# Performance work log

Measured on AMD Instinct MI355X. Metric: run time of the kernel, lower is better.

Reference implementation:

```python
import jax, jax.numpy as jnp
import numpy as np

N = 20000        # nodes
E = 320000       # directed edges (before self-loops)
HEADS = 4
IN_DIM = 256
HID = [256, 128]
ZD = [128, 64]
S = 10           # num_samples in reparameterize
REAL_MIN = 2.2e-10
THETA_MAX = 1000.0
KMIN, KMAX = 0.1, 1000.0
SLOPE = 0.2      # GATConv leaky_relu negative_slope


def setup_inputs() -> dict:
    key = jax.random.key(0)
    ks = jax.random.split(key, 24)
    f32 = jnp.float32
    def p(k, shape, scale):
        return jax.random.normal(k, shape, dtype=f32) * scale
    inp = {}
    inp["x"] = jax.random.normal(ks[0], (N, IN_DIM), dtype=f32)
    inp["edge_index"] = jax.random.randint(ks[1], (2, E), 0, N)
    # layer 0: GAT 256 -> 4 heads x 64 (concat = 256)
    inp["gatW0"] = p(ks[2], (HID[0], IN_DIM), 0.06)
    inp["asrc0"] = p(ks[3], (HEADS, HID[0] // HEADS), 0.1)
    inp["adst0"] = p(ks[4], (HEADS, HID[0] // HEADS), 0.1)
    inp["gatb0"] = p(ks[5], (HID[0],), 0.02)
    inp["fcW0"] = p(ks[6], (ZD[0], HID[0]), 0.06)
    inp["fcb0"] = p(ks[7], (ZD[0],), 0.02)
    inp["shW0"] = p(ks[8], (ZD[0], ZD[0]), 0.08)
    inp["shb0"] = p(ks[9], (ZD[0],), 0.02)
    inp["scW0"] = p(ks[10], (ZD[0], ZD[0]), 0.08)
    inp["scb0"] = p(ks[11], (ZD[0],), 0.02)
    # layer 1: GAT 256 -> 4 heads x 32 (concat = 128)
    inp["gatW1"] = p(ks[12], (HID[1], HID[0]), 0.06)
    inp["asrc1"] = p(ks[13], (HEADS, HID[1] // HEADS), 0.1)
    inp["adst1"] = p(ks[14], (HEADS, HID[1] // HEADS), 0.1)
    inp["gatb1"] = p(ks[15], (HID[1],), 0.02)
    inp["fcW1"] = p(ks[16], (ZD[1], HID[1]), 0.06)
    inp["fcb1"] = p(ks[17], (ZD[1],), 0.02)
    inp["shW1"] = p(ks[18], (ZD[1], ZD[1]), 0.08)
    inp["shb1"] = p(ks[19], (ZD[1],), 0.02)
    inp["scW1"] = p(ks[20], (ZD[1], ZD[1]), 0.08)
    inp["scb1"] = p(ks[21], (ZD[1],), 0.02)
    # Weibull reparameterization noise eps ~ U(0,1), shape (S, z_dim, N)
    inp["eps0"] = jax.random.uniform(ks[22], (S, ZD[0], N), dtype=f32)
    inp["eps1"] = jax.random.uniform(ks[23], (S, ZD[1], N), dtype=f32)
    return inp


def _gat(x, src, dst, W, a_src, a_dst, b):
    """PyG GATConv (shared lin, concat heads, add_self_loops done by caller)."""
    n = x.shape[0]
    xw = (x @ W.T).reshape(n, HEADS, -1)            # [N, H, C]
    s = (xw * a_src[None]).sum(-1)                  # [N, H] alpha_src
    d = (xw * a_dst[None]).sum(-1)                  # [N, H] alpha_dst
    e = s[src] + d[dst]                             # [E, H]
    e = jnp.where(e > 0, e, SLOPE * e)              # leaky_relu
    m = jax.lax.stop_gradient(jax.ops.segment_max(e, dst, num_segments=n))
    ex = jnp.exp(e - m[dst])
    den = jax.ops.segment_sum(ex, dst, num_segments=n)
    alpha = ex / (den[dst] + 1e-16)                 # segment softmax over in-edges
    out = jax.ops.segment_sum(alpha[:, :, None] * xw[src], dst, num_segments=n)
    return out.reshape(n, -1) + b                   # [N, H*C]


def _reparam(k, l, eps):
    # theta = l * (-log(max(1-eps, real_min)))^(1/k), mean over samples, clamp
    lm = jnp.log(jnp.maximum(1.0 - eps, REAL_MIN))  # [S, z, N]
    theta = l[None] * jnp.power(-lm, 1.0 / k[None])
    return jnp.clip(theta.mean(0), REAL_MIN, THETA_MAX)


def _right(h, Wk, bk, Wl, bl, eps):
    k = jnp.clip(jax.nn.softplus(h @ Wk.T + bk).T, KMIN, KMAX)      # [z, N]
    l = jnp.maximum(jax.nn.softplus(h @ Wl.T + bl).T, REAL_MIN)     # [z, N]
    l = l / jnp.exp(jax.lax.lgamma(1.0 + 1.0 / k))
    return _reparam(k, l, eps), k, l


def reference(x, edge_index, gatW0, asrc0, adst0, gatb0, fcW0, fcb0, shW0, shb0,
              scW0, scb0, gatW1, asrc1, adst1, gatb1, fcW1, fcb1, shW1, shb1,
              scW1, scb1, eps0, eps1):
    n = x.shape[0]
    loops = jnp.arange(n)
    src = jnp.concatenate([edge_index[0], loops])   # GATConv add_self_loops
    dst = jnp.concatenate([edge_index[1], loops])
    h0 = _gat(x, src, dst, gatW0, asrc0, adst0, gatb0)
    z0 = jax.nn.softplus(h0 @ fcW0.T + fcb0)
    h1 = _gat(h0, src, dst, gatW1, asrc1, adst1, gatb1)
    z1 = jax.nn.softplus(h1 @ fcW1.T + fcb1)
    theta1, k1, l1 = _right(z1, shW1, shb1, scW1, scb1, eps1)
    theta0, k0, l0 = _right(z0, shW0, shb0, scW0, scb0, eps0)
    return (theta0, theta1, k0, k1, l0, l1)
```

## Files before the change

### kernel.cpp

```cpp
#include <hip/hip_runtime.h>
#include <math.h>

#define N_NODES 20000
#define E_EDGES 320000
#define NHEADS 4
#define RMIN 2.2e-10f
#define THETA_MAX 1000.0f
#define SLOPE 0.2f

__device__ __forceinline__ float softplus_f(float x) {
    return fmaxf(x, 0.0f) + log1pf(expf(-fabsf(x)));
}

__global__ __launch_bounds__(256) void count_kernel(const int* __restrict__ dst,
                                                    int* __restrict__ deg) {
    int e = blockIdx.x * 256 + threadIdx.x;
    if (e < E_EDGES) atomicAdd(&deg[dst[e]], 1);
}

__global__ __launch_bounds__(256) void scan_kernel(const int* __restrict__ deg,
                                                   int* __restrict__ rowptr,
                                                   int* __restrict__ cursor) {
    __shared__ int part[256];
    int t = threadIdx.x;
    const int CH = (N_NODES + 255) / 256;
    int base = t * CH;
    int sum = 0;
    for (int i = 0; i < CH; ++i) {
        int idx = base + i;
        if (idx < N_NODES) sum += deg[idx];
    }
    part[t] = sum;
    __syncthreads();
    for (int off = 1; off < 256; off <<= 1) {
        int v = (t >= off) ? part[t - off] : 0;
        __syncthreads();
        part[t] += v;
        __syncthreads();
    }
    int run = (t == 0) ? 0 : part[t - 1];
    for (int i = 0; i < CH; ++i) {
        int idx = base + i;
        if (idx < N_NODES) {
            rowptr[idx] = run;
            cursor[idx] = run;
            run += deg[idx];
        }
    }
    if (t == 255) rowptr[N_NODES] = run;
}

__global__ __launch_bounds__(256) void scatter_kernel(const int* __restrict__ src,
                                                      const int* __restrict__ dst,
                                                      int* __restrict__ cursor,
                                                      int* __restrict__ csr) {
    int e = blockIdx.x * 256 + threadIdx.x;
    if (e < E_EDGES) {
        int p = atomicAdd(&cursor[dst[e]], 1);
        csr[p] = src[e];
    }
}

template <int MODE, bool TRANS>
__global__ __launch_bounds__(256) void gemm_kernel(const float* __restrict__ A,
                                                   const float* __restrict__ W,
                                                   const float* __restrict__ bias,
                                                   float* __restrict__ out,
                                                   int M, int K, int NO) {
    __shared__ float As[16][68];
    __shared__ float Bs[16][68];
    int tid = threadIdx.x;
    int tx = tid & 15, ty = tid >> 4;
    int bm = blockIdx.x * 64;
    int bn = blockIdx.y * 64;
    float acc[4][4] = {};
    for (int k0 = 0; k0 < K; k0 += 16) {
        {
            int m = tid >> 2;
            int kk0 = (tid & 3) * 4;
            int row = bm + m;
            float4 v = make_float4(0.f, 0.f, 0.f, 0.f);
            if (row < M) v = *(const float4*)(A + (size_t)row * K + k0 + kk0);
            As[kk0 + 0][m] = v.x; As[kk0 + 1][m] = v.y;
            As[kk0 + 2][m] = v.z; As[kk0 + 3][m] = v.w;
        }
        {
            int o = tid >> 2;
            int kk0 = (tid & 3) * 4;
            float4 v = *(const float4*)(W + (size_t)(bn + o) * K + k0 + kk0);
            Bs[kk0 + 0][o] = v.x; Bs[kk0 + 1][o] = v.y;
            Bs[kk0 + 2][o] = v.z; Bs[kk0 + 3][o] = v.w;
        }
        __syncthreads();
#pragma unroll
        for (int kk = 0; kk < 16; ++kk) {
            float a[4], b[4];
            *(float4*)a = *(const float4*)(&As[kk][ty * 4]);
            *(float4*)b = *(const float4*)(&Bs[kk][tx * 4]);
#pragma unroll
            for (int i = 0; i < 4; ++i)
#pragma unroll
                for (int j = 0; j < 4; ++j) acc[i][j] += a[i] * b[j];
        }
        __syncthreads();
    }
    int r0 = bm + ty * 4;
    int c0 = bn + tx * 4;
    float bv[4] = {0.f, 0.f, 0.f, 0.f};
    if (MODE != 0) *(float4*)bv = *(const float4*)(bias + c0);
    float vals[4][4];
#pragma unroll
    for (int i = 0; i < 4; ++i)
#pragma unroll
        for (int j = 0; j < 4; ++j) {
            float v = acc[i][j];
            if (MODE == 1) v = softplus_f(v + bv[j]);
            else if (MODE == 2) { v = softplus_f(v + bv[j]); v = fminf(fmaxf(v, 0.1f), 1000.0f); }
            else if (MODE == 3) { v = fmaxf(softplus_f(v + bv[j]), RMIN); }
            vals[i][j] = v;
        }
    if (!TRANS) {
#pragma unroll
        for (int i = 0; i < 4; ++i) {
            int row = r0 + i;
            if (row < M) *(float4*)(out + (size_t)row * NO + c0) = *(float4*)vals[i];
        }
    } else {
        if (r0 + 3 < M) {
#pragma unroll
            for (int j = 0; j < 4; ++j) {
                float col[4] = {vals[0][j], vals[1][j], vals[2][j], vals[3][j]};
                *(float4*)(out + (size_t)(c0 + j) * M + r0) = *(float4*)col;
            }
        } else {
#pragma unroll
            for (int i = 0; i < 4; ++i) {
                int row = r0 + i;
                if (row < M)
#pragma unroll
                    for (int j = 0; j < 4; ++j) out[(size_t)(c0 + j) * M + row] = vals[i][j];
            }
        }
    }
}

template <int F, int CPER>
__global__ __launch_bounds__(256) void sd_kernel(const float* __restrict__ xw,
                                                 const float* __restrict__ asrc,
                                                 const float* __restrict__ adst,
                                                 float* __restrict__ s,
                                                 float* __restrict__ d) {
    int wave = threadIdx.x >> 6;
    int lane = threadIdx.x & 63;
    int n = blockIdx.x * 4 + wave;
    if (n >= N_NODES) return;
    float ss[NHEADS] = {0, 0, 0, 0}, dd[NHEADS] = {0, 0, 0, 0};
#pragma unroll
    for (int j = 0; j < F / 64; ++j) {
        int c = j * 64 + lane;
        int h = c / CPER;
        int cc = c % CPER;
        float v = xw[(size_t)n * F + c];
        ss[h] += v * asrc[h * CPER + cc];
        dd[h] += v * adst[h * CPER + cc];
    }
#pragma unroll
    for (int off = 32; off > 0; off >>= 1) {
#pragma unroll
        for (int h = 0; h < NHEADS; ++h) {
            ss[h] += __shfl_xor(ss[h], off, 64);
            dd[h] += __shfl_xor(dd[h], off, 64);
        }
    }
    if (lane == 0) {
#pragma unroll
        for (int h = 0; h < NHEADS; ++h) {
            s[n * NHEADS + h] = ss[h];
            d[n * NHEADS + h] = dd[h];
        }
    }
}

template <int F, int CPER>
__global__ __launch_bounds__(256) void agg_kernel(const float* __restrict__ xw,
                                                  const float* __restrict__ s,
                                                  const float* __restrict__ d,
                                                  const int* __restrict__ rowptr,
                                                  const int* __restrict__ csr,
                                                  const float* __restrict__ bias,
                                                  float* __restrict__ out) {
    int wave = threadIdx.x >> 6;
    int lane = threadIdx.x & 63;
    int n = blockIdx.x * 4 + wave;
    if (n >= N_NODES) return;
    constexpr int J = F / 64;
    float dh[NHEADS], shh[NHEADS];
#pragma unroll
    for (int h = 0; h < NHEADS; ++h) {
        dh[h] = d[n * NHEADS + h];
        shh[h] = s[n * NHEADS + h];
    }
    float den[NHEADS], w[NHEADS], acc[J];
#pragma unroll
    for (int h = 0; h < NHEADS; ++h) {
        float e = shh[h] + dh[h];
        e = e > 0.f ? e : SLOPE * e;
        w[h] = expf(e);
        den[h] = w[h];
    }
#pragma unroll
    for (int j = 0; j < J; ++j) {
        int c = j * 64 + lane;
        acc[j] = w[c / CPER] * xw[(size_t)n * F + c];
    }
    int beg = rowptr[n], end = rowptr[n + 1];
    for (int idx = beg; idx < end; ++idx) {
        int srcn = csr[idx];
#pragma unroll
        for (int h = 0; h < NHEADS; ++h) {
            float e = s[srcn * NHEADS + h] + dh[h];
            e = e > 0.f ? e : SLOPE * e;
            w[h] = expf(e);
            den[h] += w[h];
        }
#pragma unroll
        for (int j = 0; j < J; ++j) {
            int c = j * 64 + lane;
            acc[j] += w[c / CPER] * xw[(size_t)srcn * F + c];
        }
    }
#pragma unroll
    for (int j = 0; j < J; ++j) {
        int c = j * 64 + lane;
        out[(size_t)n * F + c] = acc[j] / (den[c / CPER] + 1e-16f) + bias[c];
    }
}

__global__ __launch_bounds__(256) void theta_kernel(const float* __restrict__ eps,
                                                    const float* __restrict__ kptr,
                                                    float* __restrict__ lptr,
                                                    float* __restrict__ theta, int ZN) {
    int i = blockIdx.x * 256 + threadIdx.x;
    if (i >= ZN) return;
    float k = kptr[i];
    float invk = 1.0f / k;
    float lg = expf(lgammaf(1.0f + invk));
    float l = lptr[i] / lg;
    lptr[i] = l;
    float acc = 0.0f;
#pragma unroll
    for (int ss = 0; ss < 10; ++ss) {
        float u = eps[(size_t)ss * ZN + i];
        float v = -logf(fmaxf(1.0f - u, RMIN));
        acc += exp2f(log2f(v) * invk);
    }
    float th = l * acc * 0.1f;
    th = fminf(fmaxf(th, RMIN), THETA_MAX);
    theta[i] = th;
}

extern "C" void kernel_launch(void* const* d_in, const int* in_sizes, int n_in,
                              void* d_out, int out_size, void* d_ws, size_t ws_size,
                              hipStream_t stream) {
    const float* x     = (const float*)d_in[0];
    const int*   eidx  = (const int*)d_in[1];
    const float* gatW0 = (const float*)d_in[2];
    const float* asrc0 = (const float*)d_in[3];
    const float* adst0 = (const float*)d_in[4];
    const float* gatb0 = (const float*)d_in[5];
    const float* fcW0  = (const float*)d_in[6];
    const float* fcb0  = (const float*)d_in[7];
    const float* shW0  = (const float*)d_in[8];
    const float* shb0  = (const float*)d_in[9];
    const float* scW0  = (const float*)d_in[10];
    const float* scb0  = (const float*)d_in[11];
    const float* gatW1 = (const float*)d_in[12];
    const float* asrc1 = (const float*)d_in[13];
    const float* adst1 = (const float*)d_in[14];
    const float* gatb1 = (const float*)d_in[15];
    const float* fcW1  = (const float*)d_in[16];
    const float* fcb1  = (const float*)d_in[17];
    const float* shW1  = (const float*)d_in[18];
    const float* shb1  = (const float*)d_in[19];
    const float* scW1  = (const float*)d_in[20];
    const float* scb1  = (const float*)d_in[21];
    const float* eps0  = (const float*)d_in[22];
    const float* eps1  = (const float*)d_in[23];

    const int* e_src = eidx;
    const int* e_dst = eidx + E_EDGES;

    size_t off = 0;
    auto carve = [&](size_t elems) {
        void* p = (char*)d_ws + off;
        off += ((elems * 4 + 255) / 256) * 256;
        return p;
    };
    float* xw0 = (float*)carve(20000u * 256);
    float* h0  = (float*)carve(20000u * 256);
    float* z0  = (float*)carve(20000u * 128);
    float* xw1 = (float*)carve(20000u * 128);
    float* h1  = (float*)carve(20000u * 128);
    float* z1  = (float*)carve(20000u * 64);
    float* s0  = (float*)carve(20000u * 4);
    float* d0  = (float*)carve(20000u * 4);
    float* s1  = (float*)carve(20000u * 4);
    float* d1  = (float*)carve(20000u * 4);
    int* deg    = (int*)carve(20000);
    int* rowptr = (int*)carve(20001);
    int* cursor = (int*)carve(20000);
    int* csr    = (int*)carve(E_EDGES);

    float* out    = (float*)d_out;
    float* theta0 = out;
    float* theta1 = out + 2560000;
    float* k0     = out + 3840000;
    float* k1     = out + 6400000;
    float* l0     = out + 7680000;
    float* l1     = out + 10240000;

    const int M = N_NODES;
    dim3 blk(256);

    (void)hipMemsetAsync(deg, 0, N_NODES * sizeof(int), stream);
    count_kernel<<<(E_EDGES + 255) / 256, blk, 0, stream>>>(e_dst, deg);
    scan_kernel<<<1, blk, 0, stream>>>(deg, rowptr, cursor);
    scatter_kernel<<<(E_EDGES + 255) / 256, blk, 0, stream>>>(e_src, e_dst, cursor, csr);

    gemm_kernel<0, false><<<dim3(313, 4), blk, 0, stream>>>(x, gatW0, nullptr, xw0, M, 256, 256);
    sd_kernel<256, 64><<<5000, blk, 0, stream>>>(xw0, asrc0, adst0, s0, d0);
    agg_kernel<256, 64><<<5000, blk, 0, stream>>>(xw0, s0, d0, rowptr, csr, gatb0, h0);
    gemm_kernel<1, false><<<dim3(313, 2), blk, 0, stream>>>(h0, fcW0, fcb0, z0, M, 256, 128);

    gemm_kernel<0, false><<<dim3(313, 2), blk, 0, stream>>>(h0, gatW1, nullptr, xw1, M, 256, 128);
    sd_kernel<128, 32><<<5000, blk, 0, stream>>>(xw1, asrc1, adst1, s1, d1);
    agg_kernel<128, 32><<<5000, blk, 0, stream>>>(xw1, s1, d1, rowptr, csr, gatb1, h1);
    gemm_kernel<1, false><<<dim3(313, 1), blk, 0, stream>>>(h1, fcW1, fcb1, z1, M, 128, 64);

    gemm_kernel<2, true><<<dim3(313, 2), blk, 0, stream>>>(z0, shW0, shb0, k0, M, 128, 128);
    gemm_kernel<3, true><<<dim3(313, 2), blk, 0, stream>>>(z0, scW0, scb0, l0, M, 128, 128);
    gemm_kernel<2, true><<<dim3(313, 1), blk, 0, stream>>>(z1, shW1, shb1, k1, M, 64, 64);
    gemm_kernel<3, true><<<dim3(313, 1), blk, 0, stream>>>(z1, scW1, scb1, l1, M, 64, 64);

    theta_kernel<<<(2560000 + 255) / 256, blk, 0, stream>>>(eps0, k0, l0, theta0, 2560000);
    theta_kernel<<<(1280000 + 255) / 256, blk, 0, stream>>>(eps1, k1, l1, theta1, 1280000);
}
```

Measured before the change: 684.0 us.

## Precompute per-edge attention weights in separate kernel and unroll aggregation by two

Adds an edge-weight kernel that computes leaky-relu and exp attention weights for every CSR edge and self-loop once, storing them as float4 per edge. The scatter step now also records each edge's destination in CSR order. The aggregation kernel reads these precomputed weights instead of recomputing exp per head on every lane, and processes two neighbours per iteration to expose more memory-level parallelism. In exchange it adds an extra launch and about 5 MB of weight traffic per layer.

```diff
diff --git a/kernel.cpp b/kernel.cpp
--- a/kernel.cpp
+++ b/kernel.cpp
@@ -53,12 +53,45 @@
 __global__ __launch_bounds__(256) void scatter_kernel(const int* __restrict__ src,
                                                       const int* __restrict__ dst,
                                                       int* __restrict__ cursor,
-                                                      int* __restrict__ csr) {
+                                                      int* __restrict__ csr,
+                                                      int* __restrict__ dnd) {
     int e = blockIdx.x * 256 + threadIdx.x;
     if (e < E_EDGES) {
-        int p = atomicAdd(&cursor[dst[e]], 1);
+        int dn = dst[e];
+        int p = atomicAdd(&cursor[dn], 1);
         csr[p] = src[e];
-    }
+        dnd[p] = dn;
+    }
+}
+
+__global__ __launch_bounds__(256) void eweight_kernel(const int* __restrict__ csr,
+                                                      const int* __restrict__ dnd,
+                                                      const float* __restrict__ s,
+                                                      const float* __restrict__ d,
+                                                      float* __restrict__ w4,
+                                                      float* __restrict__ wself) {
+    int p = blockIdx.x * 256 + threadIdx.x;
+    if (p >= E_EDGES + N_NODES) return;
+    int sn, dn;
+    float* outp;
+    if (p < E_EDGES) {
+        sn = csr[p];
+        dn = dnd[p];
+        outp = w4 + 4 * (size_t)p;
+    } else {
+        sn = p - E_EDGES;
+        dn = sn;
+        outp = wself + 4 * (size_t)sn;
+    }
+    float4 sv = *(const float4*)(s + 4 * (size_t)sn);
+    float4 dv = *(const float4*)(d + 4 * (size_t)dn);
+    float4 wv;
+    float e;
+    e = sv.x + dv.x; e = e > 0.f ? e : SLOPE * e; wv.x = expf(e);
+    e = sv.y + dv.y; e = e > 0.f ? e : SLOPE * e; wv.y = expf(e);
+    e = sv.z + dv.z; e = e > 0.f ? e : SLOPE * e; wv.z = expf(e);
+    e = sv.w + dv.w; e = e > 0.f ? e : SLOPE * e; wv.w = expf(e);
+    *(float4*)outp = wv;
 }
 
 template <int MODE, bool TRANS>
@@ -181,12 +214,23 @@
     }
 }
 
+template <int CPER>
+__device__ __forceinline__ float pick_w(float4 w, int j, int lane) {
+    if constexpr (CPER == 64) {
+        return j == 0 ? w.x : (j == 1 ? w.y : (j == 2 ? w.z : w.w));
+    } else {
+        float lo = (j == 0) ? w.x : w.z;
+        float hi = (j == 0) ? w.y : w.w;
+        return (lane & 32) ? hi : lo;
+    }
+}
+
 template <int F, int CPER>
 __global__ __launch_bounds__(256) void agg_kernel(const float* __restrict__ xw,
-                                                  const float* __restrict__ s,
-                                                  const float* __restrict__ d,
                                                   const int* __restrict__ rowptr,
                                                   const int* __restrict__ csr,
+                                                  const float* __restrict__ w4,
+                                                  const float* __restrict__ wself,
                                                   const float* __restrict__ bias,
                                                   float* __restrict__ out) {
     int wave = threadIdx.x >> 6;
@@ -194,45 +238,57 @@
     int n = blockIdx.x * 4 + wave;
     if (n >= N_NODES) return;
     constexpr int J = F / 64;
-    float dh[NHEADS], shh[NHEADS];
-#pragma unroll
-    for (int h = 0; h < NHEADS; ++h) {
-        dh[h] = d[n * NHEADS + h];
-        shh[h] = s[n * NHEADS + h];
-    }
-    float den[NHEADS], w[NHEADS], acc[J];
-#pragma unroll
-    for (int h = 0; h < NHEADS; ++h) {
-        float e = shh[h] + dh[h];
-        e = e > 0.f ? e : SLOPE * e;
-        w[h] = expf(e);
-        den[h] = w[h];
-    }
+
+    float4 wl = *(const float4*)(wself + 4 * (size_t)n);
+    float den[NHEADS] = {wl.x, wl.y, wl.z, wl.w};
+    float acc[J];
 #pragma unroll
     for (int j = 0; j < J; ++j) {
         int c = j * 64 + lane;
-        acc[j] = w[c / CPER] * xw[(size_t)n * F + c];
-    }
+        acc[j] = pick_w<CPER>(wl, j, lane) * xw[(size_t)n * F + c];
+    }
+
     int beg = rowptr[n], end = rowptr[n + 1];
-    for (int idx = beg; idx < end; ++idx) {
-        int srcn = csr[idx];
-#pragma unroll
-        for (int h = 0; h < NHEADS; ++h) {
-            float e = s[srcn * NHEADS + h] + dh[h];
-            e = e > 0.f ? e : SLOPE * e;
-            w[h] = expf(e);
-            den[h] += w[h];
-        }
+    int idx = beg;
+    for (; idx + 2 <= end; idx += 2) {
+        int sa = csr[idx], sb = csr[idx + 1];
+        float4 wa = *(const float4*)(w4 + 4 * (size_t)idx);
+        float4 wb = *(const float4*)(w4 + 4 * (size_t)(idx + 1));
+        den[0] += wa.x + wb.x;
+        den[1] += wa.y + wb.y;
+        den[2] += wa.z + wb.z;
+        den[3] += wa.w + wb.w;
+        const float* ra = xw + (size_t)sa * F;
+        const float* rb = xw + (size_t)sb * F;
 #pragma unroll
         for (int j = 0; j < J; ++j) {
             int c = j * 64 + lane;
-            acc[j] += w[c / CPER] * xw[(size_t)srcn * F + c];
-        }
-    }
+            acc[j] += pick_w<CPER>(wa, j, lane) * ra[c];
+            acc[j] += pick_w<CPER>(wb, j, lane) * rb[c];
+        }
+    }
+    if (idx < end) {
+        int sa = csr[idx];
+        float4 wa = *(const float4*)(w4 + 4 * (size_t)idx);
+        den[0] += wa.x;
+        den[1] += wa.y;
+        den[2] += wa.z;
+        den[3] += wa.w;
+        const float* ra = xw + (size_t)sa * F;
+#pragma unroll
+        for (int j = 0; j < J; ++j) {
+            int c = j * 64 + lane;
+            acc[j] += pick_w<CPER>(wa, j, lane) * ra[c];
+        }
+    }
+
 #pragma unroll
     for (int j = 0; j < J; ++j) {
         int c = j * 64 + lane;
-        out[(size_t)n * F + c] = acc[j] / (den[c / CPER] + 1e-16f) + bias[c];
+        float dv;
+        if constexpr (CPER == 64) dv = den[j];
+        else dv = (lane & 32) ? den[2 * j + 1] : den[2 * j];
+        out[(size_t)n * F + c] = acc[j] / (dv + 1e-16f) + bias[c];
     }
 }
 
@@ -310,6 +366,9 @@
     int* rowptr = (int*)carve(20001);
     int* cursor = (int*)carve(20000);
     int* csr    = (int*)carve(E_EDGES);
+    int* dnd    = (int*)carve(E_EDGES);
+    float* w4    = (float*)carve((size_t)E_EDGES * 4);
+    float* wself = (float*)carve(20000u * 4);
 
     float* out    = (float*)d_out;
     float* theta0 = out;
@@ -321,20 +380,23 @@
 
     const int M = N_NODES;
     dim3 blk(256);
+    const int EW_BLOCKS = (E_EDGES + N_NODES + 255) / 256;
 
     (void)hipMemsetAsync(deg, 0, N_NODES * sizeof(int), stream);
     count_kernel<<<(E_EDGES + 255) / 256, blk, 0, stream>>>(e_dst, deg);
     scan_kernel<<<1, blk, 0, stream>>>(deg, rowptr, cursor);
-    scatter_kernel<<<(E_EDGES + 255) / 256, blk, 0, stream>>>(e_src, e_dst, cursor, csr);
+    scatter_kernel<<<(E_EDGES + 255) / 256, blk, 0, stream>>>(e_src, e_dst, cursor, csr, dnd);
 
     gemm_kernel<0, false><<<dim3(313, 4), blk, 0, stream>>>(x, gatW0, nullptr, xw0, M, 256, 256);
     sd_kernel<256, 64><<<5000, blk, 0, stream>>>(xw0, asrc0, adst0, s0, d0);
-    agg_kernel<256, 64><<<5000, blk, 0, stream>>>(xw0, s0, d0, rowptr, csr, gatb0, h0);
+    eweight_kernel<<<EW_BLOCKS, blk, 0, stream>>>(csr, dnd, s0, d0, w4, wself);
+    agg_kernel<256, 64><<<5000, blk, 0, stream>>>(xw0, rowptr, csr, w4, wself, gatb0, h0);
     gemm_kernel<1, false><<<dim3(313, 2), blk, 0, stream>>>(h0, fcW0, fcb0, z0, M, 256, 128);
 
     gemm_kernel<0, false><<<dim3(313, 2), blk, 0, stream>>>(h0, gatW1, nullptr, xw1, M, 256, 128);
     sd_kernel<128, 32><<<5000, blk, 0, stream>>>(xw1, asrc1, adst1, s1, d1);
-    agg_kernel<128, 32><<<5000, blk, 0, stream>>>(xw1, s1, d1, rowptr, csr, gatb1, h1);
+    eweight_kernel<<<EW_BLOCKS, blk, 0, stream>>>(csr, dnd, s1, d1, w4, wself);
+    agg_kernel<128, 32><<<5000, blk, 0, stream>>>(xw1, rowptr, csr, w4, wself, gatb1, h1);
     gemm_kernel<1, false><<<dim3(313, 1), blk, 0, stream>>>(h1, fcW1, fcb1, z1, M, 128, 64);
 
     gemm_kernel<2, true><<<dim3(313, 2), blk, 0, stream>>>(z0, shW0, shb0, k0, M, 128, 128);
```

Measured after the change: 658.3 us. 1.04x faster.
